# Performance work log

Measured on AMD Instinct MI355X. Metric: run time of the kernel, lower is better.

## Reference

```python
import jax, jax.numpy as jnp
import numpy as np
import math

N_HEAD = 16
ROPE_BASE = 10000.0


def _rope(xh):
    # xh: [B, H, T, D]; rotate full head dim using half-split (GPT-NeoX style)
    B, H, T, D = xh.shape
    theta = 1.0 / (ROPE_BASE ** (jnp.arange(0, D, 2, dtype=jnp.float32) / D))  # [D/2]
    idx_theta = jnp.arange(T, dtype=jnp.float32)[:, None] * theta[None, :]      # [T, D/2]
    idx_theta2 = jnp.concatenate([idx_theta, idx_theta], axis=1)                 # [T, D]
    cos = jnp.cos(idx_theta2)[None, None]                                        # [1,1,T,D]
    sin = jnp.sin(idx_theta2)[None, None]
    d2 = D // 2
    neg_half = jnp.concatenate([-xh[..., d2:], xh[..., :d2]], axis=-1)
    return xh * cos + neg_half * sin


def setup_inputs() -> dict:
    key = jax.random.key(0)
    k1, k2, k3 = jax.random.split(key, 3)
    B, T, C = 2, 2048, 2048
    x = jax.random.normal(k1, (B, T, C), dtype=jnp.float32)
    w_attn = jax.random.normal(k2, (C, 3 * C), dtype=jnp.float32) * (1.0 / math.sqrt(C))
    w_proj = jax.random.normal(k3, (C, C), dtype=jnp.float32) * (1.0 / math.sqrt(C))
    return {"x": x, "w_attn": w_attn, "w_proj": w_proj}


def reference(x, w_attn, w_proj):
    B, T, C = x.shape
    H = N_HEAD
    D = C // H
    qkv = x @ w_attn                                   # [B,T,3C]
    q, k, v = jnp.split(qkv, 3, axis=-1)
    # [B,T,C] -> [B,H,T,D]
    to_heads = lambda t: t.reshape(B, T, H, D).transpose(0, 2, 1, 3)
    q, k, v = to_heads(q), to_heads(k), to_heads(v)
    q = _rope(q)
    k = _rope(k)
    att = jnp.einsum('bhqd,bhkd->bhqk', q, k) * (1.0 / math.sqrt(D))
    causal = jnp.tril(jnp.ones((T, T), dtype=bool))
    att = jnp.where(causal[None, None], att, -jnp.inf)
    att = jax.nn.softmax(att, axis=-1)
    y = jnp.einsum('bhqk,bhkd->bhqd', att, v)          # [B,H,T,D]
    y = y.transpose(0, 2, 1, 3).reshape(B, T, C)
    return y @ w_proj
```

## Files before the change

kernel.cpp:

```cpp
#include <hip/hip_runtime.h>
#include <hip/hip_bf16.h>
#include <math.h>

typedef __bf16 bf16;
typedef __bf16 bf16x8 __attribute__((ext_vector_type(8)));
typedef float f32x4 __attribute__((ext_vector_type(4)));
typedef float f32x16 __attribute__((ext_vector_type(16)));
typedef unsigned int u32x2 __attribute__((ext_vector_type(2)));
typedef unsigned int u32x4 __attribute__((ext_vector_type(4)));

#define MFMA16(a, b, c) __builtin_amdgcn_mfma_f32_16x16x32_bf16((a), (b), (c), 0, 0, 0)
#define MFMA32(a, b, c) __builtin_amdgcn_mfma_f32_32x32x16_bf16((a), (b), (c), 0, 0, 0)

static constexpr int Bsz = 2, Tsz = 2048, Csz = 2048, Hn = 16, Dh = 128;
static constexpr float ATTN_SCALE = 0.08838834764831845f;

__device__ __forceinline__ void gld16(const void* src, void* dst) {
    __builtin_amdgcn_global_load_lds((__attribute__((address_space(1))) void*)src,
                                     (__attribute__((address_space(3))) void*)dst,
                                     16, 0, 0);
}

__device__ __forceinline__ unsigned cvt_pk_bf16(float lo, float hi) {
    unsigned r;
    asm("v_cvt_pk_bf16_f32 %0, %1, %2" : "=v"(r) : "v"(lo), "v"(hi));
    return r;
}

__device__ __forceinline__ bf16x8 make_pfrag(float p0, float p1, float p2, float p3,
                                             float p4, float p5, float p6, float p7) {
    unsigned a0 = cvt_pk_bf16(p0, p1), a1 = cvt_pk_bf16(p2, p3);
    unsigned b0 = cvt_pk_bf16(p4, p5), b1 = cvt_pk_bf16(p6, p7);
    asm volatile("v_permlane32_swap_b32 %0, %1" : "+v"(a0), "+v"(b0));
    asm volatile("v_permlane32_swap_b32 %0, %1" : "+v"(a1), "+v"(b1));
    u32x4 w = {a0, a1, b0, b1};
    return __builtin_bit_cast(bf16x8, w);
}

__global__ __launch_bounds__(256) void cast_x_kernel(const float* __restrict__ x,
                                                     bf16* __restrict__ o, int n8) {
    int i = blockIdx.x * 256 + threadIdx.x;
    if (i >= n8) return;
    const float4* x4 = (const float4*)x;
    float4 a = x4[2 * i], b = x4[2 * i + 1];
    bf16x8 v;
    v[0] = (bf16)a.x; v[1] = (bf16)a.y; v[2] = (bf16)a.z; v[3] = (bf16)a.w;
    v[4] = (bf16)b.x; v[5] = (bf16)b.y; v[6] = (bf16)b.z; v[7] = (bf16)b.w;
    ((bf16x8*)o)[i] = v;
}

template <typename TIN>
__global__ __launch_bounds__(256) void transpose_cast_kernel(const TIN* __restrict__ in,
                                                             bf16* __restrict__ out,
                                                             int R, int Cc) {
    __shared__ float tile[64][65];
    const int tx = threadIdx.x, ty = threadIdx.y;
    in  += (size_t)blockIdx.z * R * Cc;
    out += (size_t)blockIdx.z * R * Cc;
    const int c0 = blockIdx.x * 64, r0 = blockIdx.y * 64;
#pragma unroll
    for (int j = 0; j < 16; ++j) {
        int rr = ty + j * 4;
        tile[rr][tx] = (float)in[(size_t)(r0 + rr) * Cc + c0 + tx];
    }
    __syncthreads();
#pragma unroll
    for (int j = 0; j < 16; ++j) {
        int cc = ty + j * 4;
        out[(size_t)(c0 + cc) * R + r0 + tx] = (bf16)tile[tx][cc];
    }
}

__global__ __launch_bounds__(256) void cossin_kernel(float2* __restrict__ cs) {
    int idx = blockIdx.x * 256 + threadIdx.x;
    int t = idx >> 6, i = idx & 63;
    float theta = 1.0f / powf(10000.0f, (float)(2 * i) / 128.0f);
    float ang = (float)t * theta;
    cs[idx] = make_float2(cosf(ang), sinf(ang));
}

__global__ __launch_bounds__(512, 2)
void gemm384_qkv(const bf16* __restrict__ A, const bf16* __restrict__ Bt,
                 bf16* __restrict__ Oq, bf16* __restrict__ Ok, bf16* __restrict__ Ov,
                 const float2* __restrict__ cs, int K) {
    __shared__ bf16 sA[2][128 * 64];
    __shared__ bf16 sB[2][384 * 64];
    const int tid = threadIdx.x, lane = tid & 63, wid = tid >> 6;
    const int wm = wid >> 2, wn = wid & 3;
    const int lo16 = lane & 15, hi4 = lane >> 4;

    const int cpx = gridDim.x >> 3;
    const int swz = (blockIdx.x & 7) * cpx + (blockIdx.x >> 3);
    const int by = swz & 31;
    const int bx = swz >> 5;
    const int row0 = by << 7, col0 = bx * 384;

    const int srow = tid >> 3;
    const int swzoff = (((tid & 7) ^ ((tid >> 3) & 7)) << 3);
    const bf16* srcA = A  + (size_t)(row0 + srow) * K + swzoff;
    const bf16* srcB = Bt + (size_t)(col0 + srow) * K + swzoff;
    const size_t K64 = (size_t)K * 64;
    char* const ldsA = (char*)&sA[0][0];
    char* const ldsB = (char*)&sB[0][0];
    const int wuo = wid << 10;

    auto issueA = [&](int c, int kt) {
        const bf16* s = srcA + (size_t)kt * 64;
        gld16(s,       ldsA + c * 16384 + 0    + wuo);
        gld16(s + K64, ldsA + c * 16384 + 8192 + wuo);
    };
    auto issueB = [&](int c, int kt, int u) {
        const bf16* s = srcB + (size_t)kt * 64 + (size_t)(2 * u) * K64;
        gld16(s,       ldsB + c * 49152 + u * 16384 + 0    + wuo);
        gld16(s + K64, ldsB + c * 49152 + u * 16384 + 8192 + wuo);
    };
    auto ldF = [&](const char* buf, int row, int ks) {
        return *(const bf16x8*)(buf + row * 128 + ((((ks << 2) + hi4) ^ (row & 7)) << 4));
    };

    const int arow = (wm << 6) + lo16;
    const int brow = (wn << 4) + lo16;

    f32x4 acc[4][6] = {};
    const int nkt = K >> 6;

    issueA(0, 0); issueB(0, 0, 0); issueB(0, 0, 1); issueB(0, 0, 2);
    __syncthreads();

    for (int kt = 0; kt < nkt; ++kt) {
        const int c = kt & 1;
        const char* bufA = ldsA + c * 16384;
        const char* bufB = ldsB + c * 49152;
        if (kt + 1 < nkt) {
            issueA(c ^ 1, kt + 1);
            issueB(c ^ 1, kt + 1, 0);
            issueB(c ^ 1, kt + 1, 1);
            issueB(c ^ 1, kt + 1, 2);
        }
        bf16x8 af[4][2], bq[6][2];
#pragma unroll
        for (int i = 0; i < 4; ++i) {
            af[i][0] = ldF(bufA, arow + (i << 4), 0);
            af[i][1] = ldF(bufA, arow + (i << 4), 1);
        }
#pragma unroll
        for (int j = 0; j < 6; ++j) {
            bq[j][0] = ldF(bufB, brow + (j << 6), 0);
            bq[j][1] = ldF(bufB, brow + (j << 6), 1);
        }
        __builtin_amdgcn_s_setprio(1);
#pragma unroll
        for (int ks = 0; ks < 2; ++ks)
#pragma unroll
            for (int i = 0; i < 4; ++i)
#pragma unroll
                for (int j = 0; j < 6; ++j)
                    acc[i][j] = MFMA16(af[i][ks], bq[j][ks], acc[i][j]);
        __builtin_amdgcn_s_setprio(0);
        __syncthreads();
    }

    const int d = (wn << 4) + lo16;
#pragma unroll
    for (int p = 0; p < 3; ++p) {
        const int gcb = col0 + (p << 7);
        const int seg = gcb >> 11;
        const int hb = (gcb >> 7) & 15;
        if (seg < 2) {
            bf16* dst0 = (seg == 0) ? Oq : Ok;
            const float qs = (seg == 0) ? ATTN_SCALE : 1.0f;
#pragma unroll
            for (int mi = 0; mi < 4; ++mi)
#pragma unroll
                for (int r = 0; r < 4; ++r) {
                    const int gm = row0 + (wm << 6) + (mi << 4) + (hi4 << 2) + r;
                    const int b = gm >> 11, t = gm & 2047;
                    const float2 csv = cs[t * 64 + d];
                    bf16* drow = dst0 + ((((size_t)b * Hn + hb) * Tsz + t) << 7);
                    const float vlo = acc[mi][2 * p][r];
                    const float vhi = acc[mi][2 * p + 1][r];
                    drow[d]      = (bf16)((vlo * csv.x - vhi * csv.y) * qs);
                    drow[d + 64] = (bf16)((vhi * csv.x + vlo * csv.y) * qs);
                }
        } else {
#pragma unroll
            for (int mi = 0; mi < 4; ++mi)
#pragma unroll
                for (int r = 0; r < 4; ++r) {
                    const int gm = row0 + (wm << 6) + (mi << 4) + (hi4 << 2) + r;
                    const int b = gm >> 11, t = gm & 2047;
                    bf16* drow = Ov + ((((size_t)b * Hn + hb) * Tsz + t) << 7);
                    drow[d]      = (bf16)acc[mi][2 * p][r];
                    drow[d + 64] = (bf16)acc[mi][2 * p + 1][r];
                }
        }
    }
}

__global__ __launch_bounds__(512, 2)
void gemm256_proj(const bf16* __restrict__ A, const bf16* __restrict__ Bt,
                  float* __restrict__ Cf, int K) {
    __shared__ bf16 sA[2][128 * 64];
    __shared__ bf16 sB[2][256 * 64];
    const int tid = threadIdx.x, lane = tid & 63, wid = tid >> 6;
    const int wm = wid >> 2, wn = wid & 3;
    const int lo16 = lane & 15, hi4 = lane >> 4;
    const int N = 2048;

    const int cpx = gridDim.x >> 3;
    const int swz = (blockIdx.x & 7) * cpx + (blockIdx.x >> 3);
    const int by = swz & 31;
    const int bx = swz >> 5;
    const int row0 = by << 7, col0 = bx << 8;

    const int srow = tid >> 3;
    const int swzoff = (((tid & 7) ^ ((tid >> 3) & 7)) << 3);
    const bf16* srcA = A  + (size_t)(row0 + srow) * K + swzoff;
    const bf16* srcB = Bt + (size_t)(col0 + srow) * K + swzoff;
    const size_t K64 = (size_t)K * 64;
    char* const ldsA = (char*)&sA[0][0];
    char* const ldsB = (char*)&sB[0][0];
    const int wuo = wid << 10;

    auto issueA = [&](int c, int kt) {
        const bf16* s = srcA + (size_t)kt * 64;
        gld16(s,       ldsA + c * 16384 + 0    + wuo);
        gld16(s + K64, ldsA + c * 16384 + 8192 + wuo);
    };
    auto issueB = [&](int c, int kt, int u) {
        const bf16* s = srcB + (size_t)kt * 64 + (size_t)(2 * u) * K64;
        gld16(s,       ldsB + c * 32768 + u * 16384 + 0    + wuo);
        gld16(s + K64, ldsB + c * 32768 + u * 16384 + 8192 + wuo);
    };
    auto ldF = [&](const char* buf, int row, int ks) {
        return *(const bf16x8*)(buf + row * 128 + ((((ks << 2) + hi4) ^ (row & 7)) << 4));
    };

    const int arow = (wm << 6) + lo16;
    const int brow = (wn << 4) + lo16;

    f32x4 acc[4][4] = {};
    const int nkt = K >> 6;

    issueA(0, 0); issueB(0, 0, 0); issueB(0, 0, 1);
    __syncthreads();

    for (int kt = 0; kt < nkt; ++kt) {
        const int c = kt & 1;
        const char* bufA = ldsA + c * 16384;
        const char* bufB = ldsB + c * 32768;
        if (kt + 1 < nkt) {
            issueA(c ^ 1, kt + 1);
            issueB(c ^ 1, kt + 1, 0);
            issueB(c ^ 1, kt + 1, 1);
        }
        bf16x8 af[4][2], bq[4][2];
#pragma unroll
        for (int i = 0; i < 4; ++i) {
            af[i][0] = ldF(bufA, arow + (i << 4), 0);
            af[i][1] = ldF(bufA, arow + (i << 4), 1);
        }
#pragma unroll
        for (int j = 0; j < 4; ++j) {
            bq[j][0] = ldF(bufB, brow + (j << 6), 0);
            bq[j][1] = ldF(bufB, brow + (j << 6), 1);
        }
        __builtin_amdgcn_s_setprio(1);
#pragma unroll
        for (int ks = 0; ks < 2; ++ks)
#pragma unroll
            for (int i = 0; i < 4; ++i)
#pragma unroll
                for (int j = 0; j < 4; ++j)
                    acc[i][j] = MFMA16(af[i][ks], bq[j][ks], acc[i][j]);
        __builtin_amdgcn_s_setprio(0);
        __syncthreads();
    }

#pragma unroll
    for (int mi = 0; mi < 4; ++mi)
#pragma unroll
        for (int r = 0; r < 4; ++r) {
            const int gm = row0 + (wm << 6) + (mi << 4) + (hi4 << 2) + r;
            float* crow = Cf + (size_t)gm * N + col0 + (wn << 4) + lo16;
#pragma unroll
            for (int nj = 0; nj < 4; ++nj)
                crow[nj << 6] = acc[mi][nj][r];
        }
}

__device__ __forceinline__ void stage_tile(const bf16* __restrict__ Kb,
                                           const bf16* __restrict__ Vtb,
                                           bf16* sKc, bf16* sVc, int k0, int tid) {
#pragma unroll
    for (int c = 0; c < 4; ++c) {
        const int off = (c << 12) + (tid << 4);
        const int row = off >> 8, u = (off >> 4) & 15;
        gld16(Kb + (size_t)(k0 + row) * Dh + ((u ^ (row & 7)) << 3), (char*)sKc + off);
        const int dv = off >> 7, uv = (off >> 4) & 7;
        gld16(Vtb + (size_t)dv * Tsz + k0 + ((uv ^ (dv & 7)) << 3), (char*)sVc + off);
    }
}

__global__ __launch_bounds__(256, 2)
void attn_kernel(const bf16* __restrict__ Q, const bf16* __restrict__ K,
                 const bf16* __restrict__ Vt, bf16* __restrict__ Y) {
    __shared__ bf16 sK[2][64 * 128];
    __shared__ bf16 sV[2][128 * 64];
    const int tid = threadIdx.x, lane = tid & 63, wv = tid >> 6;
    const int lo32 = lane & 31, hl = lane >> 5;

    const int i = blockIdx.x;
    const int g = i >> 5;
    const int bh = i & 31;
    const int t = (i < 256) ? (15 - g) : (g - 8);
    const int b = bh >> 4, h = bh & 15;

    const int q0 = t << 7;
    const int q0w = q0 + (wv << 5);
    const int qg = q0w + lo32;

    const bf16* Kb  = K  + (size_t)bh * (Tsz * Dh);
    const bf16* Vtb = Vt + (size_t)bh * (Tsz * Dh);
    const bf16* Qp  = Q  + (size_t)bh * (Tsz * Dh) + (size_t)qg * Dh;

    bf16x8 qf[8];
#pragma unroll
    for (int kc = 0; kc < 8; ++kc)
        qf[kc] = *(const bf16x8*)(Qp + (kc << 4) + (hl << 3));

    float m = -1e30f, lsum = 0.f;
    f32x16 o[4] = {};

    const int nt_block = 2 * t + 2;
    const int nt_warp = ((q0w + 31) >> 6) + 1;

    stage_tile(Kb, Vtb, &sK[0][0], &sV[0][0], 0, tid);

    int cur = 0;
    for (int kt = 0; kt < nt_block; ++kt) {
        __syncthreads();
        if (kt + 1 < nt_block)
            stage_tile(Kb, Vtb, &sK[cur ^ 1][0], &sV[cur ^ 1][0], (kt + 1) << 6, tid);
        if (kt < nt_warp) {
            const int k0 = kt << 6;
            const bf16* kbuf = &sK[cur][0];
            const bf16* vbuf = &sV[cur][0];
            f32x16 s0 = {}, s1 = {};
            const int swk = lo32 & 7;
            __builtin_amdgcn_s_setprio(1);
#pragma unroll
            for (int kc = 0; kc < 8; ++kc) {
                bf16x8 kf0 = *(const bf16x8*)((const char*)kbuf + lo32 * 256 +
                              ((((kc << 1) + hl) ^ swk) << 4));
                s0 = MFMA32(kf0, qf[kc], s0);
                bf16x8 kf1 = *(const bf16x8*)((const char*)kbuf + (32 + lo32) * 256 +
                              ((((kc << 1) + hl) ^ swk) << 4));
                s1 = MFMA32(kf1, qf[kc], s1);
            }
            __builtin_amdgcn_s_setprio(0);

            const bool bnd = (k0 + 63 > q0w);
            if (bnd) {
#pragma unroll
                for (int r = 0; r < 16; ++r) {
                    const int kl = (r & 3) + ((r >> 2) << 3) + (hl << 2);
                    if (k0 + kl > qg)      s0[r] = -1e30f;
                    if (k0 + 32 + kl > qg) s1[r] = -1e30f;
                }
            }
            float pm = s0[0];
#pragma unroll
            for (int r = 1; r < 16; ++r) pm = fmaxf(pm, s0[r]);
#pragma unroll
            for (int r = 0; r < 16; ++r) pm = fmaxf(pm, s1[r]);
            pm = fmaxf(pm, __shfl_xor(pm, 32));

            if (__any(pm > m + 8.0f)) {
                const float mn = fmaxf(m, pm);
                const float sc = __expf(m - mn);
                m = mn;
                lsum *= sc;
#pragma unroll
                for (int db = 0; db < 4; ++db)
#pragma unroll
                    for (int r = 0; r < 16; ++r) o[db][r] *= sc;
            }
            float rs = 0.f;
            if (bnd) {
#pragma unroll
                for (int r = 0; r < 16; ++r) {
                    float e0 = (s0[r] > -1e29f) ? __expf(s0[r] - m) : 0.f;
                    float e1 = (s1[r] > -1e29f) ? __expf(s1[r] - m) : 0.f;
                    s0[r] = e0; s1[r] = e1; rs += e0 + e1;
                }
            } else {
#pragma unroll
                for (int r = 0; r < 16; ++r) {
                    float e0 = __expf(s0[r] - m);
                    float e1 = __expf(s1[r] - m);
                    s0[r] = e0; s1[r] = e1; rs += e0 + e1;
                }
            }
            rs += __shfl_xor(rs, 32);
            lsum += rs;

            bf16x8 pb0 = make_pfrag(s0[0], s0[1], s0[2],  s0[3],  s0[4],  s0[5],  s0[6],  s0[7]);
            bf16x8 pb1 = make_pfrag(s0[8], s0[9], s0[10], s0[11], s0[12], s0[13], s0[14], s0[15]);
            bf16x8 pb2 = make_pfrag(s1[0], s1[1], s1[2],  s1[3],  s1[4],  s1[5],  s1[6],  s1[7]);
            bf16x8 pb3 = make_pfrag(s1[8], s1[9], s1[10], s1[11], s1[12], s1[13], s1[14], s1[15]);

            __builtin_amdgcn_s_setprio(1);
#pragma unroll
            for (int db = 0; db < 4; ++db) {
                const int rd = (db << 5) + lo32;
                const char* vrow = (const char*)vbuf + rd * 128;
                const int sw = rd & 7;
                bf16x8 v0 = *(const bf16x8*)(vrow + (((0 + hl) ^ sw) << 4));
                o[db] = MFMA32(v0, pb0, o[db]);
                bf16x8 v1 = *(const bf16x8*)(vrow + (((2 + hl) ^ sw) << 4));
                o[db] = MFMA32(v1, pb1, o[db]);
                bf16x8 v2 = *(const bf16x8*)(vrow + (((4 + hl) ^ sw) << 4));
                o[db] = MFMA32(v2, pb2, o[db]);
                bf16x8 v3 = *(const bf16x8*)(vrow + (((6 + hl) ^ sw) << 4));
                o[db] = MFMA32(v3, pb3, o[db]);
            }
            __builtin_amdgcn_s_setprio(0);
        }
        cur ^= 1;
    }

    const float inv = 1.0f / lsum;
    const size_t rowoff = ((size_t)b * Tsz + qg) * (size_t)Csz + (size_t)h * 128;
#pragma unroll
    for (int db = 0; db < 4; ++db)
#pragma unroll
        for (int gg = 0; gg < 4; ++gg) {
            unsigned w0 = cvt_pk_bf16(o[db][4 * gg + 0] * inv, o[db][4 * gg + 1] * inv);
            unsigned w1 = cvt_pk_bf16(o[db][4 * gg + 2] * inv, o[db][4 * gg + 3] * inv);
            u32x2 w = {w0, w1};
            *(u32x2*)(Y + rowoff + (db << 5) + (gg << 3) + (hl << 2)) = w;
        }
}

extern "C" void kernel_launch(void* const* d_in, const int* in_sizes, int n_in,
                              void* d_out, int out_size, void* d_ws, size_t ws_size,
                              hipStream_t stream) {
    const float* x      = (const float*)d_in[0];
    const float* w_attn = (const float*)d_in[1];
    const float* w_proj = (const float*)d_in[2];
    float* out = (float*)d_out;

    char* ws = (char*)d_ws;
    bf16* Xb  = (bf16*)(ws);
    bf16* Wat = (bf16*)(ws + 16777216);
    bf16* Wpt = (bf16*)(ws + 41943040);
    bf16* Qr  = (bf16*)(ws + 50331648);
    bf16* Kr  = (bf16*)(ws + 67108864);
    bf16* Vb  = (bf16*)(ws + 83886080);
    bf16* Vt  = (bf16*)(ws + 100663296);
    bf16* Yb  = (bf16*)(ws + 117440512);
    float2* cs = (float2*)(ws + 134217728);

    cast_x_kernel<<<4096, 256, 0, stream>>>(x, Xb, (Bsz * Tsz * Csz) / 8);
    transpose_cast_kernel<float><<<dim3(96, 32, 1), dim3(64, 4), 0, stream>>>(w_attn, Wat, 2048, 6144);
    transpose_cast_kernel<float><<<dim3(32, 32, 1), dim3(64, 4), 0, stream>>>(w_proj, Wpt, 2048, 2048);
    cossin_kernel<<<512, 256, 0, stream>>>(cs);

    gemm384_qkv<<<512, 512, 0, stream>>>(Xb, Wat, Qr, Kr, Vb, cs, 2048);
    transpose_cast_kernel<bf16><<<dim3(2, 32, 32), dim3(64, 4), 0, stream>>>(Vb, Vt, 2048, 128);

    attn_kernel<<<dim3(512), 256, 0, stream>>>(Qr, Kr, Vt, Yb);

    gemm256_proj<<<256, 512, 0, stream>>>(Yb, Wpt, out, 2048);
}
```

Baseline: 275.8 us.

## Shrink QKV GEMM tile to 128x128 and split-phase pipeline both GEMMs

The QKV GEMM moves from 128x384 tiles with 512 blocks to 128x128 tiles with 1536 blocks and a higher occupancy bound. Both GEMMs now split each K-step into two MFMA phases and issue the global-to-LDS loads in pieces between them, with explicit vmcnt/lgkmcnt waits and raw barriers. The goal is more blocks per CU and overlap of loads with MFMA work. The cost is more A-tile reloads, since each tile now reuses data across fewer columns, and fragile hand-counted waitcnt logic that can race if the counts are wrong.

New measurement: 253.0 us. 1.09x faster.

```diff
diff --git a/kernel.cpp b/kernel.cpp
--- a/kernel.cpp
+++ b/kernel.cpp
@@ -79,12 +79,12 @@
     cs[idx] = make_float2(cosf(ang), sinf(ang));
 }
 
-__global__ __launch_bounds__(512, 2)
-void gemm384_qkv(const bf16* __restrict__ A, const bf16* __restrict__ Bt,
+__global__ __launch_bounds__(512, 4)
+void gemm128_qkv(const bf16* __restrict__ A, const bf16* __restrict__ Bt,
                  bf16* __restrict__ Oq, bf16* __restrict__ Ok, bf16* __restrict__ Ov,
                  const float2* __restrict__ cs, int K) {
     __shared__ bf16 sA[2][128 * 64];
-    __shared__ bf16 sB[2][384 * 64];
+    __shared__ bf16 sB[2][128 * 64];
     const int tid = threadIdx.x, lane = tid & 63, wid = tid >> 6;
     const int wm = wid >> 2, wn = wid & 3;
     const int lo16 = lane & 15, hi4 = lane >> 4;
@@ -93,7 +93,7 @@
     const int swz = (blockIdx.x & 7) * cpx + (blockIdx.x >> 3);
     const int by = swz & 31;
     const int bx = swz >> 5;
-    const int row0 = by << 7, col0 = bx * 384;
+    const int row0 = by << 7, col0 = bx << 7;
 
     const int srow = tid >> 3;
     const int swzoff = (((tid & 7) ^ ((tid >> 3) & 7)) << 3);
@@ -109,10 +109,10 @@
         gld16(s,       ldsA + c * 16384 + 0    + wuo);
         gld16(s + K64, ldsA + c * 16384 + 8192 + wuo);
     };
-    auto issueB = [&](int c, int kt, int u) {
-        const bf16* s = srcB + (size_t)kt * 64 + (size_t)(2 * u) * K64;
-        gld16(s,       ldsB + c * 49152 + u * 16384 + 0    + wuo);
-        gld16(s + K64, ldsB + c * 49152 + u * 16384 + 8192 + wuo);
+    auto issueB = [&](int c, int kt) {
+        const bf16* s = srcB + (size_t)kt * 64;
+        gld16(s,       ldsB + c * 16384 + 0    + wuo);
+        gld16(s + K64, ldsB + c * 16384 + 8192 + wuo);
     };
     auto ldF = [&](const char* buf, int row, int ks) {
         return *(const bf16x8*)(buf + row * 128 + ((((ks << 2) + hi4) ^ (row & 7)) << 4));
@@ -121,79 +121,86 @@
     const int arow = (wm << 6) + lo16;
     const int brow = (wn << 4) + lo16;
 
-    f32x4 acc[4][6] = {};
+    f32x4 acc[4][2] = {};
     const int nkt = K >> 6;
 
-    issueA(0, 0); issueB(0, 0, 0); issueB(0, 0, 1); issueB(0, 0, 2);
-    __syncthreads();
+    issueA(0, 0); issueB(0, 0);
+    if (nkt > 1) issueA(1, 1);
+    asm volatile("s_waitcnt vmcnt(2)" ::: "memory");
+    __builtin_amdgcn_s_barrier();
 
     for (int kt = 0; kt < nkt; ++kt) {
         const int c = kt & 1;
         const char* bufA = ldsA + c * 16384;
-        const char* bufB = ldsB + c * 49152;
-        if (kt + 1 < nkt) {
-            issueA(c ^ 1, kt + 1);
-            issueB(c ^ 1, kt + 1, 0);
-            issueB(c ^ 1, kt + 1, 1);
-            issueB(c ^ 1, kt + 1, 2);
-        }
-        bf16x8 af[4][2], bq[6][2];
+        const char* bufB = ldsB + c * 16384;
+        bf16x8 af[4][2], bq[2];
 #pragma unroll
         for (int i = 0; i < 4; ++i) {
             af[i][0] = ldF(bufA, arow + (i << 4), 0);
             af[i][1] = ldF(bufA, arow + (i << 4), 1);
         }
-#pragma unroll
-        for (int j = 0; j < 6; ++j) {
-            bq[j][0] = ldF(bufB, brow + (j << 6), 0);
-            bq[j][1] = ldF(bufB, brow + (j << 6), 1);
-        }
+        bq[0] = ldF(bufB, brow, 0);
+        bq[1] = ldF(bufB, brow, 1);
+        if (kt + 1 < nkt) issueB(c ^ 1, kt + 1);
+        __builtin_amdgcn_s_barrier();
+        asm volatile("s_waitcnt lgkmcnt(0)" ::: "memory");
+        __builtin_amdgcn_sched_barrier(0);
         __builtin_amdgcn_s_setprio(1);
 #pragma unroll
         for (int ks = 0; ks < 2; ++ks)
 #pragma unroll
             for (int i = 0; i < 4; ++i)
-#pragma unroll
-                for (int j = 0; j < 6; ++j)
-                    acc[i][j] = MFMA16(af[i][ks], bq[j][ks], acc[i][j]);
+                acc[i][0] = MFMA16(af[i][ks], bq[ks], acc[i][0]);
         __builtin_amdgcn_s_setprio(0);
-        __syncthreads();
-    }
-
+        __builtin_amdgcn_s_barrier();
+        bq[0] = ldF(bufB, brow + 64, 0);
+        bq[1] = ldF(bufB, brow + 64, 1);
+        if (kt + 2 < nkt) issueA(c, kt + 2);
+        __builtin_amdgcn_s_barrier();
+        asm volatile("s_waitcnt lgkmcnt(0)" ::: "memory");
+        __builtin_amdgcn_sched_barrier(0);
+        __builtin_amdgcn_s_setprio(1);
+#pragma unroll
+        for (int ks = 0; ks < 2; ++ks)
+#pragma unroll
+            for (int i = 0; i < 4; ++i)
+                acc[i][1] = MFMA16(af[i][ks], bq[ks], acc[i][1]);
+        __builtin_amdgcn_s_setprio(0);
+        if (kt + 2 < nkt)      asm volatile("s_waitcnt vmcnt(2)" ::: "memory");
+        else if (kt + 1 < nkt) asm volatile("s_waitcnt vmcnt(0)" ::: "memory");
+        __builtin_amdgcn_s_barrier();
+    }
+
+    const int seg = col0 >> 11;
+    const int hb = (col0 >> 7) & 15;
     const int d = (wn << 4) + lo16;
-#pragma unroll
-    for (int p = 0; p < 3; ++p) {
-        const int gcb = col0 + (p << 7);
-        const int seg = gcb >> 11;
-        const int hb = (gcb >> 7) & 15;
-        if (seg < 2) {
-            bf16* dst0 = (seg == 0) ? Oq : Ok;
-            const float qs = (seg == 0) ? ATTN_SCALE : 1.0f;
-#pragma unroll
-            for (int mi = 0; mi < 4; ++mi)
-#pragma unroll
-                for (int r = 0; r < 4; ++r) {
-                    const int gm = row0 + (wm << 6) + (mi << 4) + (hi4 << 2) + r;
-                    const int b = gm >> 11, t = gm & 2047;
-                    const float2 csv = cs[t * 64 + d];
-                    bf16* drow = dst0 + ((((size_t)b * Hn + hb) * Tsz + t) << 7);
-                    const float vlo = acc[mi][2 * p][r];
-                    const float vhi = acc[mi][2 * p + 1][r];
-                    drow[d]      = (bf16)((vlo * csv.x - vhi * csv.y) * qs);
-                    drow[d + 64] = (bf16)((vhi * csv.x + vlo * csv.y) * qs);
-                }
-        } else {
-#pragma unroll
-            for (int mi = 0; mi < 4; ++mi)
-#pragma unroll
-                for (int r = 0; r < 4; ++r) {
-                    const int gm = row0 + (wm << 6) + (mi << 4) + (hi4 << 2) + r;
-                    const int b = gm >> 11, t = gm & 2047;
-                    bf16* drow = Ov + ((((size_t)b * Hn + hb) * Tsz + t) << 7);
-                    drow[d]      = (bf16)acc[mi][2 * p][r];
-                    drow[d + 64] = (bf16)acc[mi][2 * p + 1][r];
-                }
-        }
+    if (seg < 2) {
+        bf16* dst0 = (seg == 0) ? Oq : Ok;
+        const float qs = (seg == 0) ? ATTN_SCALE : 1.0f;
+#pragma unroll
+        for (int mi = 0; mi < 4; ++mi)
+#pragma unroll
+            for (int r = 0; r < 4; ++r) {
+                const int gm = row0 + (wm << 6) + (mi << 4) + (hi4 << 2) + r;
+                const int b = gm >> 11, t = gm & 2047;
+                const float2 csv = cs[t * 64 + d];
+                bf16* drow = dst0 + ((((size_t)b * Hn + hb) * Tsz + t) << 7);
+                const float vlo = acc[mi][0][r];
+                const float vhi = acc[mi][1][r];
+                drow[d]      = (bf16)((vlo * csv.x - vhi * csv.y) * qs);
+                drow[d + 64] = (bf16)((vhi * csv.x + vlo * csv.y) * qs);
+            }
+    } else {
+#pragma unroll
+        for (int mi = 0; mi < 4; ++mi)
+#pragma unroll
+            for (int r = 0; r < 4; ++r) {
+                const int gm = row0 + (wm << 6) + (mi << 4) + (hi4 << 2) + r;
+                const int b = gm >> 11, t = gm & 2047;
+                bf16* drow = Ov + ((((size_t)b * Hn + hb) * Tsz + t) << 7);
+                drow[d]      = (bf16)acc[mi][0][r];
+                drow[d + 64] = (bf16)acc[mi][1][r];
+            }
     }
 }
 
@@ -243,38 +250,62 @@
     const int nkt = K >> 6;
 
     issueA(0, 0); issueB(0, 0, 0); issueB(0, 0, 1);
-    __syncthreads();
+    if (nkt > 1) { issueA(1, 1); issueB(1, 1, 0); }
+    asm volatile("s_waitcnt vmcnt(4)" ::: "memory");
+    __builtin_amdgcn_s_barrier();
 
     for (int kt = 0; kt < nkt; ++kt) {
         const int c = kt & 1;
         const char* bufA = ldsA + c * 16384;
         const char* bufB = ldsB + c * 32768;
-        if (kt + 1 < nkt) {
-            issueA(c ^ 1, kt + 1);
-            issueB(c ^ 1, kt + 1, 0);
-            issueB(c ^ 1, kt + 1, 1);
-        }
-        bf16x8 af[4][2], bq[4][2];
+        bf16x8 af[4][2], bq[2][2];
 #pragma unroll
         for (int i = 0; i < 4; ++i) {
             af[i][0] = ldF(bufA, arow + (i << 4), 0);
             af[i][1] = ldF(bufA, arow + (i << 4), 1);
         }
 #pragma unroll
-        for (int j = 0; j < 4; ++j) {
+        for (int j = 0; j < 2; ++j) {
             bq[j][0] = ldF(bufB, brow + (j << 6), 0);
             bq[j][1] = ldF(bufB, brow + (j << 6), 1);
         }
+        if (kt + 1 < nkt) issueB(c ^ 1, kt + 1, 1);
+        __builtin_amdgcn_s_barrier();
+        asm volatile("s_waitcnt lgkmcnt(0)" ::: "memory");
+        __builtin_amdgcn_sched_barrier(0);
         __builtin_amdgcn_s_setprio(1);
 #pragma unroll
         for (int ks = 0; ks < 2; ++ks)
 #pragma unroll
             for (int i = 0; i < 4; ++i)
 #pragma unroll
-                for (int j = 0; j < 4; ++j)
+                for (int j = 0; j < 2; ++j)
                     acc[i][j] = MFMA16(af[i][ks], bq[j][ks], acc[i][j]);
         __builtin_amdgcn_s_setprio(0);
-        __syncthreads();
+        if (kt + 1 < nkt) asm volatile("s_waitcnt vmcnt(6)" ::: "memory");
+        else              asm volatile("s_waitcnt vmcnt(0)" ::: "memory");
+        __builtin_amdgcn_s_barrier();
+#pragma unroll
+        for (int j = 0; j < 2; ++j) {
+            bq[j][0] = ldF(bufB, brow + ((j + 2) << 6), 0);
+            bq[j][1] = ldF(bufB, brow + ((j + 2) << 6), 1);
+        }
+        if (kt + 2 < nkt) { issueA(c, kt + 2); issueB(c, kt + 2, 0); }
+        __builtin_amdgcn_s_barrier();
+        asm volatile("s_waitcnt lgkmcnt(0)" ::: "memory");
+        __builtin_amdgcn_sched_barrier(0);
+        __builtin_amdgcn_s_setprio(1);
+#pragma unroll
+        for (int ks = 0; ks < 2; ++ks)
+#pragma unroll
+            for (int i = 0; i < 4; ++i)
+#pragma unroll
+                for (int j = 0; j < 2; ++j)
+                    acc[i][j + 2] = MFMA16(af[i][ks], bq[j][ks], acc[i][j + 2]);
+        __builtin_amdgcn_s_setprio(0);
+        if (kt + 2 < nkt)      asm volatile("s_waitcnt vmcnt(6)" ::: "memory");
+        else if (kt + 1 < nkt) asm volatile("s_waitcnt vmcnt(2)" ::: "memory");
+        __builtin_amdgcn_s_barrier();
     }
 
 #pragma unroll
@@ -467,7 +498,7 @@
     transpose_cast_kernel<float><<<dim3(32, 32, 1), dim3(64, 4), 0, stream>>>(w_proj, Wpt, 2048, 2048);
     cossin_kernel<<<512, 256, 0, stream>>>(cs);
 
-    gemm384_qkv<<<512, 512, 0, stream>>>(Xb, Wat, Qr, Kr, Vb, cs, 2048);
+    gemm128_qkv<<<1536, 512, 0, stream>>>(Xb, Wat, Qr, Kr, Vb, cs, 2048);
     transpose_cast_kernel<bf16><<<dim3(2, 32, 32), dim3(64, 4), 0, stream>>>(Vb, Vt, 2048, 128);
 
     attn_kernel<<<dim3(512), 256, 0, stream>>>(Qr, Kr, Vt, Yb);
```
